# Kernel optimization log

Hardware: AMD Instinct MI355X
Metric: run time of the kernel (lower is better)

The kernel has to match this reference:

```python
import jax, jax.numpy as jnp
import numpy as np

T0, TBAR, TPOINTS, STEP = 0.0, 2.0, 10, 0.1
N_GRID = int(np.ceil((TBAR - T0) / STEP)) + 1  # 21 internal RK4 grid points (torchdiffeq fixed-grid)
B, N, D_IN, D_HID, D_FF, D_MLP, D_OUT = 256, 100, 3, 256, 1024, 128, 2


def _linear_params(key, fan_in, fan_out):
    # torch.nn.Linear default init: U(-1/sqrt(fan_in), 1/sqrt(fan_in))
    bound = 1.0 / np.sqrt(fan_in)
    kw, kb = jax.random.split(key)
    W = jax.random.uniform(kw, (fan_out, fan_in), minval=-bound, maxval=bound, dtype=jnp.float32)
    b = jax.random.uniform(kb, (fan_out,), minval=-bound, maxval=bound, dtype=jnp.float32)
    return W, b


def setup_inputs() -> dict:
    key = jax.random.key(0)
    kx, k1, k2, k3, k4 = jax.random.split(key, 5)
    w1_W, w1_b = _linear_params(k1, D_IN, D_HID)
    w2_W, w2_b = _linear_params(k2, D_HID, D_FF)
    w3_W, w3_b = _linear_params(k3, D_FF + D_HID, D_MLP)
    out_W, out_b = _linear_params(k4, D_MLP, D_OUT)
    return dict(
        x=jax.random.normal(kx, (B, N, D_IN), dtype=jnp.float32),
        w1_W=w1_W, w1_b=w1_b,
        w2_W=w2_W, w2_b=w2_b,
        w3_W=w3_W, w3_b=w3_b,
        out_W=out_W, out_b=out_b,
        wpool_w=jnp.ones((TPOINTS,), dtype=jnp.float32),
    )


def reference(x, w1_W, w1_b, w2_W, w2_b, w3_W, w3_b, out_W, out_b, wpool_w):
    feature = jax.nn.relu(x @ w1_W.T + w1_b)              # [B, N, 256]
    gamma = feature

    def f(p):  # nmODE dynamics (time-independent)
        return -p + jnp.sin(p + gamma) ** 2

    h = jnp.float32(STEP)

    def rk4_step(y, _):
        k1 = f(y)
        k2 = f(y + 0.5 * h * k1)
        k3 = f(y + 0.5 * h * k2)
        k4 = f(y + h * k3)
        y1 = y + (h / 6.0) * (k1 + 2.0 * k2 + 2.0 * k3 + k4)
        return y1, y1

    y0 = jnp.zeros_like(feature)
    _, ys_tail = jax.lax.scan(rk4_step, y0, None, length=N_GRID - 1)
    ys = jnp.concatenate([y0[None], ys_tail], axis=0)     # [21, B, N, 256]

    # torchdiffeq interpolates fixed-grid solution linearly at the requested timepoints
    tt = np.linspace(T0, TBAR, TPOINTS)
    pos = tt / STEP
    idx = np.minimum(np.floor(pos).astype(np.int32), N_GRID - 2)
    frac = (pos - idx).astype(np.float32)[:, None, None, None]
    yt = ys[idx] * (1.0 - frac) + ys[idx + 1] * frac      # [10, B, N, 256]

    # WeightedAveragePooling over timepoints
    w = jax.nn.softmax(wpool_w)
    yt = jnp.einsum('t,tbnd->bnd', w, yt)                 # [B, N, 256]

    x2 = jax.nn.relu(feature @ w2_W.T + w2_b)             # [B, N, 1024]
    x2 = jnp.max(x2, axis=1, keepdims=True)               # [B, 1, 1024]
    x2 = jnp.broadcast_to(x2, (x2.shape[0], feature.shape[1], x2.shape[2]))
    h3 = jax.nn.relu(jnp.concatenate([x2, yt], axis=2) @ w3_W.T + w3_b)  # [B, N, 128]
    return h3 @ out_W.T + out_b                           # [B, N, 2]
```

## Files before the change

### kernel.cpp

```cpp
#include <hip/hip_runtime.h>

typedef __bf16 bf16x8 __attribute__((ext_vector_type(8)));
typedef float f32x4 __attribute__((ext_vector_type(4)));
typedef unsigned short u16x8 __attribute__((ext_vector_type(8)));

#define MFMA16(a, b, c) __builtin_amdgcn_mfma_f32_16x16x32_bf16((a), (b), (c), 0, 0, 0)

#define BN_ROWS 25600
#define INVPI 0.31830988618379067f
#define TBL_N 4096
#define TBL_SCALE 409.6f
#define TBL_STEP (10.f / 4096.f)

__device__ __forceinline__ unsigned short f2bf(float f) {
    unsigned int u = __float_as_uint(f);
    u = u + 0x7FFFu + ((u >> 16) & 1u);
    return (unsigned short)(u >> 16);
}

__device__ __forceinline__ float feval(float y, float gp) {
    float u = fmaf(y, INVPI, gp);
    float cc = __builtin_amdgcn_cosf(u);
    return fmaf(-0.5f, cc, 0.5f - y);
}

__global__ void k_prep(const float* __restrict__ w2W, const float* __restrict__ w3W,
                       const float* __restrict__ wp,
                       unsigned short* __restrict__ w2bf, unsigned short* __restrict__ w3bbf,
                       float* __restrict__ tbl, float* __restrict__ w3aT) {
    int blk = blockIdx.x;
    if (blk < 128) {
        int i = (blk * 256 + threadIdx.x) * 8;
        const float4* s4 = reinterpret_cast<const float4*>(w2W + i);
        float4 a = s4[0], b = s4[1];
        u16x8 o;
        o[0] = f2bf(a.x); o[1] = f2bf(a.y); o[2] = f2bf(a.z); o[3] = f2bf(a.w);
        o[4] = f2bf(b.x); o[5] = f2bf(b.y); o[6] = f2bf(b.z); o[7] = f2bf(b.w);
        *reinterpret_cast<u16x8*>(w2bf + i) = o;
        return;
    }
    if (blk < 144) {
        int idx = ((blk - 128) * 256 + threadIdx.x) * 8;
        int j = idx >> 8, dk = idx & 255;
        const float4* s4 = reinterpret_cast<const float4*>(w3W + j * 1280 + 1024 + dk);
        float4 a = s4[0], b = s4[1];
        u16x8 o;
        o[0] = f2bf(a.x); o[1] = f2bf(a.y); o[2] = f2bf(a.z); o[3] = f2bf(a.w);
        o[4] = f2bf(b.x); o[5] = f2bf(b.y); o[6] = f2bf(b.z); o[7] = f2bf(b.w);
        *reinterpret_cast<u16x8*>(w3bbf + idx) = o;
        return;
    }
    if (blk < 160) {
        int gid = (blk - 144) * 256 + threadIdx.x;

        float c[21];
#pragma unroll
        for (int g = 0; g < 21; ++g) c[g] = 0.f;
        {
            float wv[10];
#pragma unroll
            for (int t = 0; t < 10; ++t) wv[t] = wp[t];
            float m = wv[0];
#pragma unroll
            for (int t = 1; t < 10; ++t) m = fmaxf(m, wv[t]);
            float s = 0.f;
#pragma unroll
            for (int t = 0; t < 10; ++t) { wv[t] = __expf(wv[t] - m); s += wv[t]; }
            float inv = 1.f / s;
            const int   idxs[10]  = {0, 2, 4, 6, 8, 11, 13, 15, 17, 19};
            const float fracs[10] = {0.f, 0.22222222f, 0.44444445f, 0.6666667f, 0.8888889f,
                                     0.11111111f, 0.33333334f, 0.5555556f, 0.7777778f, 1.0f};
#pragma unroll
            for (int t = 0; t < 10; ++t) {
                float w = wv[t] * inv;
                c[idxs[t]]     += w * (1.f - fracs[t]);
                c[idxs[t] + 1] += w * fracs[t];
            }
        }

        float gamma = gid * TBL_STEP;
        float gp = gamma * INVPI;
        float y = 0.f, acc = 0.f;
#pragma unroll
        for (int st = 0; st < 20; ++st) {
            float k1 = feval(y, gp);
            float k2 = feval(fmaf(0.05f, k1, y), gp);
            float k3 = feval(fmaf(0.05f, k2, y), gp);
            float k4 = feval(fmaf(0.1f,  k3, y), gp);
            float sm = k1 + k4;
            sm = fmaf(2.f, k2, sm);
            sm = fmaf(2.f, k3, sm);
            y  = fmaf(0.1f / 6.0f, sm, y);
            acc = fmaf(c[st + 1], y, acc);
        }
        tbl[gid] = acc;
        return;
    }
    {
        int i = (blk - 160) * 256 + threadIdx.x;
        int c = i & 1023, j = i >> 10;
        w3aT[c * 128 + j] = w3W[j * 1280 + c];
    }
}

__global__ void __launch_bounds__(256) k_feat(
    const float* __restrict__ x, const float* __restrict__ w1W, const float* __restrict__ w1b,
    const float* __restrict__ tbl,
    unsigned short* __restrict__ featbf, unsigned short* __restrict__ ytbf) {

    __shared__ float tl[TBL_N];
    {
        const float4* g4 = reinterpret_cast<const float4*>(tbl);
        float4* l4 = reinterpret_cast<float4*>(tl);
#pragma unroll
        for (int r = 0; r < 4; ++r) l4[r * 256 + threadIdx.x] = g4[r * 256 + threadIdx.x];
    }
    __syncthreads();

    int tid  = blockIdx.x * 256 + threadIdx.x;
    int base = tid * 8;
    int row  = base >> 8;
    int d0   = base & 255;

    float x0 = x[row * 3 + 0], x1 = x[row * 3 + 1], x2v = x[row * 3 + 2];

    float wreg[24];
    {
        const float4* w4 = reinterpret_cast<const float4*>(w1W + d0 * 3);
#pragma unroll
        for (int q = 0; q < 6; ++q) *reinterpret_cast<float4*>(&wreg[q * 4]) = w4[q];
    }
    float bb[8];
    {
        const float4* b4 = reinterpret_cast<const float4*>(w1b + d0);
        *reinterpret_cast<float4*>(&bb[0]) = b4[0];
        *reinterpret_cast<float4*>(&bb[4]) = b4[1];
    }

    u16x8 fbv, ybv;
#pragma unroll
    for (int j = 0; j < 8; ++j) {
        float g = fmaf(x0, wreg[j * 3], fmaf(x1, wreg[j * 3 + 1], fmaf(x2v, wreg[j * 3 + 2], bb[j])));
        g = fmaxf(g, 0.f);
        fbv[j] = f2bf(g);
        float t = g * TBL_SCALE;
        int i = (int)t;
        i = (i > TBL_N - 2) ? (TBL_N - 2) : i;
        float fr = t - (float)i;
        float a = tl[i], b = tl[i + 1];
        ybv[j] = f2bf(fmaf(fr, b - a, a));
    }
    *reinterpret_cast<u16x8*>(featbf + base) = fbv;
    *reinterpret_cast<u16x8*>(ytbf + base) = ybv;
}

__global__ void __launch_bounds__(256, 2) k_gemm2max(
    const unsigned short* __restrict__ featbf, const unsigned short* __restrict__ w2bf,
    const float* __restrict__ w2bias, const float* __restrict__ w3aT,
    float* __restrict__ vpart) {

    __shared__ __align__(1024) char smem[57344];

    int p = blockIdx.x;
    int xcd = p & 7, slot = p >> 3;
    int b = xcd * 32 + (slot >> 2);
    int q = slot & 3;

    int wave = threadIdx.x >> 6, lane = threadIdx.x & 63;
    int col16 = lane & 15, krow = lane >> 4;
    int colbase = q * 256 + wave * 64;

    const unsigned short* bp = w2bf + (size_t)(colbase + col16) * 256 + krow * 8;
    bf16x8 Bcur[4], Bnxt[4];
#pragma unroll
    for (int ct = 0; ct < 4; ++ct)
        Bcur[ct] = *reinterpret_cast<const bf16x8*>(bp + ct * 4096);

    {
        const unsigned short* src = featbf + (size_t)b * 25600;
        int r_in_pair = lane >> 5;
        int chp = lane & 31;
#pragma unroll
        for (int k = 0; k < 14; ++k) {
            int pr = wave + k * 4;
            int row = pr * 2 + r_in_pair;
            if (pr < 50) {
                int ch = chp ^ (row & 7);
                const unsigned short* g = src + row * 256 + ch * 8;
                __builtin_amdgcn_global_load_lds(
                    (const __attribute__((address_space(1))) void*)g,
                    (__attribute__((address_space(3))) void*)(smem + pr * 1024),
                    16, 0, 0);
            } else {
                *reinterpret_cast<f32x4*>(smem + pr * 1024 + lane * 16) = (f32x4){0.f,0.f,0.f,0.f};
            }
        }
    }
    __syncthreads();

    int sw = (col16 & 7) << 4;

    f32x4 acc[7][4];
#pragma unroll
    for (int mt = 0; mt < 7; ++mt)
#pragma unroll
        for (int ct = 0; ct < 4; ++ct) acc[mt][ct] = (f32x4){0.f, 0.f, 0.f, 0.f};

    const char* Ab = (const char*)smem;
#pragma unroll
    for (int k0 = 0; k0 < 8; ++k0) {
        int off = (k0 * 64 + krow * 16) ^ sw;
        bf16x8 Af[7];
#pragma unroll
        for (int mt = 0; mt < 7; ++mt)
            Af[mt] = *reinterpret_cast<const bf16x8*>(Ab + (mt * 16 + col16) * 512 + off);
        if (k0 < 7) {
#pragma unroll
            for (int ct = 0; ct < 4; ++ct)
                Bnxt[ct] = *reinterpret_cast<const bf16x8*>(bp + ct * 4096 + (k0 + 1) * 32);
        }
#pragma unroll
        for (int mt = 0; mt < 7; ++mt)
#pragma unroll
            for (int ct = 0; ct < 4; ++ct)
                acc[mt][ct] = MFMA16(Af[mt], Bcur[ct], acc[mt][ct]);
#pragma unroll
        for (int ct = 0; ct < 4; ++ct) Bcur[ct] = Bnxt[ct];
    }

    float bias[4], m[4];
#pragma unroll
    for (int ct = 0; ct < 4; ++ct) {
        bias[ct] = w2bias[colbase + ct * 16 + col16];
        m[ct] = 0.f;
    }
#pragma unroll
    for (int mt = 0; mt < 7; ++mt) {
#pragma unroll
        for (int r = 0; r < 4; ++r) {
            int n = mt * 16 + krow * 4 + r;
            bool valid = n < 100;
#pragma unroll
            for (int ct = 0; ct < 4; ++ct) {
                float v = fmaxf(acc[mt][ct][r] + bias[ct], 0.f);
                if (valid) m[ct] = fmaxf(m[ct], v);
            }
        }
    }
#pragma unroll
    for (int ct = 0; ct < 4; ++ct) {
        m[ct] = fmaxf(m[ct], __shfl_xor(m[ct], 16));
        m[ct] = fmaxf(m[ct], __shfl_xor(m[ct], 32));
    }

    float* xs = (float*)smem;
    float* p0s = xs + 256;
    float* p1s = xs + 384;

    __syncthreads();
    if (lane < 16) {
#pragma unroll
        for (int ct = 0; ct < 4; ++ct)
            xs[wave * 64 + ct * 16 + lane] = m[ct];
    }
    __syncthreads();

    {
        int j = (wave & 1) * 64 + lane;
        int ch = wave >> 1;
        const float* wt = w3aT + (size_t)(q * 256 + ch * 128) * 128 + j;
        float s0 = 0.f, s1 = 0.f;
#pragma unroll 8
        for (int c = 0; c < 128; c += 2) {
            s0 = fmaf(xs[ch * 128 + c],     wt[(size_t)c * 128],       s0);
            s1 = fmaf(xs[ch * 128 + c + 1], wt[(size_t)(c + 1) * 128], s1);
        }
        float* dst = (ch == 0) ? p0s : p1s;
        dst[j] = s0 + s1;
    }
    __syncthreads();
    if (threadIdx.x < 128)
        vpart[(size_t)b * 512 + q * 128 + threadIdx.x] = p0s[threadIdx.x] + p1s[threadIdx.x];
}

__global__ void __launch_bounds__(256) k_final(
    const unsigned short* __restrict__ ytbf, const unsigned short* __restrict__ w3bbf,
    const float* __restrict__ vpart, const float* __restrict__ w3bias,
    const float* __restrict__ outW, const float* __restrict__ outb,
    float* __restrict__ out) {

    __shared__ float h3s[32][132];
    int rbase = blockIdx.x * 32;
    int wave = threadIdx.x >> 6, lane = threadIdx.x & 63;
    int col16 = lane & 15, krow = lane >> 4;

    const unsigned short* ap0 = ytbf + (size_t)(rbase + col16) * 256 + krow * 8;
    const unsigned short* ap1 = ap0 + 16 * 256;
    const unsigned short* bp0 = w3bbf + (size_t)(wave * 32 + col16) * 256 + krow * 8;
    const unsigned short* bp1 = bp0 + 16 * 256;

    f32x4 a00 = {0.f,0.f,0.f,0.f}, a01 = {0.f,0.f,0.f,0.f};
    f32x4 a10 = {0.f,0.f,0.f,0.f}, a11 = {0.f,0.f,0.f,0.f};
#pragma unroll
    for (int k0 = 0; k0 < 8; ++k0) {
        bf16x8 A0 = *reinterpret_cast<const bf16x8*>(ap0 + k0 * 32);
        bf16x8 A1 = *reinterpret_cast<const bf16x8*>(ap1 + k0 * 32);
        bf16x8 B0 = *reinterpret_cast<const bf16x8*>(bp0 + k0 * 32);
        bf16x8 B1 = *reinterpret_cast<const bf16x8*>(bp1 + k0 * 32);
        a00 = MFMA16(A0, B0, a00);
        a01 = MFMA16(A0, B1, a01);
        a10 = MFMA16(A1, B0, a10);
        a11 = MFMA16(A1, B1, a11);
    }

#pragma unroll
    for (int mt = 0; mt < 2; ++mt) {
#pragma unroll
        for (int nt = 0; nt < 2; ++nt) {
            f32x4 acc = (mt == 0) ? ((nt == 0) ? a00 : a01) : ((nt == 0) ? a10 : a11);
#pragma unroll
            for (int r = 0; r < 4; ++r) {
                int rloc  = mt * 16 + krow * 4 + r;
                int rglob = rbase + rloc;
                int bb    = rglob / 100;
                int col   = wave * 32 + nt * 16 + col16;
                const float* vp = vpart + (size_t)bb * 512;
                float vsum = (vp[col] + vp[128 + col]) + (vp[256 + col] + vp[384 + col]);
                float h = acc[r] + vsum + w3bias[col];
                h3s[rloc][col] = fmaxf(h, 0.f);
            }
        }
    }
    __syncthreads();

    int r  = threadIdx.x >> 3;
    int jg = threadIdx.x & 7;
    float p0 = 0.f, p1 = 0.f;
#pragma unroll
    for (int t = 0; t < 16; ++t) {
        int j = jg * 16 + t;
        float h = h3s[r][j];
        p0 = fmaf(h, outW[j], p0);
        p1 = fmaf(h, outW[128 + j], p1);
    }
    p0 += __shfl_xor(p0, 1); p0 += __shfl_xor(p0, 2); p0 += __shfl_xor(p0, 4);
    p1 += __shfl_xor(p1, 1); p1 += __shfl_xor(p1, 2); p1 += __shfl_xor(p1, 4);
    if (jg == 0) {
        int rg = rbase + r;
        out[rg * 2 + 0] = p0 + outb[0];
        out[rg * 2 + 1] = p1 + outb[1];
    }
}

extern "C" void kernel_launch(void* const* d_in, const int* in_sizes, int n_in,
                              void* d_out, int out_size, void* d_ws, size_t ws_size,
                              hipStream_t stream) {
    const float* x    = (const float*)d_in[0];
    const float* w1W  = (const float*)d_in[1];
    const float* w1b  = (const float*)d_in[2];
    const float* w2W  = (const float*)d_in[3];
    const float* w2b  = (const float*)d_in[4];
    const float* w3W  = (const float*)d_in[5];
    const float* w3b  = (const float*)d_in[6];
    const float* outW = (const float*)d_in[7];
    const float* outb = (const float*)d_in[8];
    const float* wp   = (const float*)d_in[9];
    float* out = (float*)d_out;

    char* ws = (char*)d_ws;
    unsigned short* featbf = (unsigned short*)(ws);
    unsigned short* ytbf   = (unsigned short*)(ws + 13107200);
    unsigned short* w2bf_  = (unsigned short*)(ws + 26214400);
    unsigned short* w3bbf_ = (unsigned short*)(ws + 26738688);
    float* tbl             = (float*)(ws + 26804224);
    float* vpart           = (float*)(ws + 26820608);
    float* w3aT            = (float*)(ws + 27344896);

    k_prep<<<672, 256, 0, stream>>>(w2W, w3W, wp, w2bf_, w3bbf_, tbl, w3aT);
    k_feat<<<3200, 256, 0, stream>>>(x, w1W, w1b, tbl, featbf, ytbf);
    k_gemm2max<<<1024, 256, 0, stream>>>(featbf, w2bf_, w2b, w3aT, vpart);
    k_final<<<800, 256, 0, stream>>>(ytbf, w3bbf_, vpart, w3b, outW, outb, out);
}
```

Measured before the change: 70.37 us.

## Fuse feature, gemm-max, and final stages into one per-batch kernel

Replaces the three kernels k_feat, k_gemm2max and k_final with a single k_batch kernel that runs one 512-thread block per batch element. Features and the interpolated ODE values are computed directly into swizzled LDS, and both GEMMs and the output projection read from there. This removes the global round trips for featbf, ytbf and vpart and two kernel launches. In exchange there are only 256 large blocks using about 140KB of LDS each, which lowers occupancy and parallelism on a GPU with many CUs.

```diff
diff --git a/kernel.cpp b/kernel.cpp
--- a/kernel.cpp
+++ b/kernel.cpp
@@ -6,7 +6,6 @@
 
 #define MFMA16(a, b, c) __builtin_amdgcn_mfma_f32_16x16x32_bf16((a), (b), (c), 0, 0, 0)
 
-#define BN_ROWS 25600
 #define INVPI 0.31830988618379067f
 #define TBL_N 4096
 #define TBL_SCALE 409.6f
@@ -103,252 +102,224 @@
     }
 }
 
-__global__ void __launch_bounds__(256) k_feat(
+__global__ void __launch_bounds__(512) k_batch(
     const float* __restrict__ x, const float* __restrict__ w1W, const float* __restrict__ w1b,
     const float* __restrict__ tbl,
-    unsigned short* __restrict__ featbf, unsigned short* __restrict__ ytbf) {
-
+    const unsigned short* __restrict__ w2bf, const float* __restrict__ w2b,
+    const float* __restrict__ w3aT, const float* __restrict__ w3b,
+    const unsigned short* __restrict__ w3bbf,
+    const float* __restrict__ outW, const float* __restrict__ outb,
+    float* __restrict__ out) {
+
+    __shared__ __align__(1024) char smemA[57344];
+    __shared__ __align__(1024) char smemY[57344];
     __shared__ float tl[TBL_N];
+    __shared__ float w1s[1024];
+    __shared__ float xs[1024];
+    __shared__ float ps[4][128];
+    __shared__ float vs[128];
+    __shared__ float ps2[4][128][2];
+
+    const int b = blockIdx.x;
+    const int t = threadIdx.x;
+
     {
         const float4* g4 = reinterpret_cast<const float4*>(tbl);
         float4* l4 = reinterpret_cast<float4*>(tl);
-#pragma unroll
-        for (int r = 0; r < 4; ++r) l4[r * 256 + threadIdx.x] = g4[r * 256 + threadIdx.x];
-    }
-    __syncthreads();
-
-    int tid  = blockIdx.x * 256 + threadIdx.x;
-    int base = tid * 8;
-    int row  = base >> 8;
-    int d0   = base & 255;
-
-    float x0 = x[row * 3 + 0], x1 = x[row * 3 + 1], x2v = x[row * 3 + 2];
-
-    float wreg[24];
-    {
-        const float4* w4 = reinterpret_cast<const float4*>(w1W + d0 * 3);
-#pragma unroll
-        for (int q = 0; q < 6; ++q) *reinterpret_cast<float4*>(&wreg[q * 4]) = w4[q];
-    }
-    float bb[8];
-    {
-        const float4* b4 = reinterpret_cast<const float4*>(w1b + d0);
-        *reinterpret_cast<float4*>(&bb[0]) = b4[0];
-        *reinterpret_cast<float4*>(&bb[4]) = b4[1];
-    }
-
-    u16x8 fbv, ybv;
-#pragma unroll
-    for (int j = 0; j < 8; ++j) {
-        float g = fmaf(x0, wreg[j * 3], fmaf(x1, wreg[j * 3 + 1], fmaf(x2v, wreg[j * 3 + 2], bb[j])));
-        g = fmaxf(g, 0.f);
-        fbv[j] = f2bf(g);
-        float t = g * TBL_SCALE;
-        int i = (int)t;
-        i = (i > TBL_N - 2) ? (TBL_N - 2) : i;
-        float fr = t - (float)i;
-        float a = tl[i], b = tl[i + 1];
-        ybv[j] = f2bf(fmaf(fr, b - a, a));
-    }
-    *reinterpret_cast<u16x8*>(featbf + base) = fbv;
-    *reinterpret_cast<u16x8*>(ytbf + base) = ybv;
-}
-
-__global__ void __launch_bounds__(256, 2) k_gemm2max(
-    const unsigned short* __restrict__ featbf, const unsigned short* __restrict__ w2bf,
-    const float* __restrict__ w2bias, const float* __restrict__ w3aT,
-    float* __restrict__ vpart) {
-
-    __shared__ __align__(1024) char smem[57344];
-
-    int p = blockIdx.x;
-    int xcd = p & 7, slot = p >> 3;
-    int b = xcd * 32 + (slot >> 2);
-    int q = slot & 3;
-
-    int wave = threadIdx.x >> 6, lane = threadIdx.x & 63;
-    int col16 = lane & 15, krow = lane >> 4;
-    int colbase = q * 256 + wave * 64;
-
-    const unsigned short* bp = w2bf + (size_t)(colbase + col16) * 256 + krow * 8;
-    bf16x8 Bcur[4], Bnxt[4];
-#pragma unroll
-    for (int ct = 0; ct < 4; ++ct)
-        Bcur[ct] = *reinterpret_cast<const bf16x8*>(bp + ct * 4096);
-
-    {
-        const unsigned short* src = featbf + (size_t)b * 25600;
-        int r_in_pair = lane >> 5;
-        int chp = lane & 31;
-#pragma unroll
-        for (int k = 0; k < 14; ++k) {
-            int pr = wave + k * 4;
-            int row = pr * 2 + r_in_pair;
-            if (pr < 50) {
-                int ch = chp ^ (row & 7);
-                const unsigned short* g = src + row * 256 + ch * 8;
-                __builtin_amdgcn_global_load_lds(
-                    (const __attribute__((address_space(1))) void*)g,
-                    (__attribute__((address_space(3))) void*)(smem + pr * 1024),
-                    16, 0, 0);
+        l4[t] = g4[t];
+        l4[t + 512] = g4[t + 512];
+        if (t < 192)
+            reinterpret_cast<float4*>(w1s)[t] = reinterpret_cast<const float4*>(w1W)[t];
+        else if (t >= 256 && t < 320)
+            reinterpret_cast<float4*>(w1s + 768)[t - 256] =
+                reinterpret_cast<const float4*>(w1b)[t - 256];
+    }
+    __syncthreads();
+
+    {
+        const float* xb = x + (size_t)b * 300;
+#pragma unroll
+        for (int i = 0; i < 7; ++i) {
+            int k = t + i * 512;
+            int row = k >> 5, ch = k & 31;
+            int byte = row * 512 + ((ch * 16) ^ ((row & 7) << 4));
+            if (row < 100) {
+                float x0 = xb[row * 3], x1 = xb[row * 3 + 1], x2 = xb[row * 3 + 2];
+                int d0 = ch * 8;
+                u16x8 fv, yv;
+#pragma unroll
+                for (int j = 0; j < 8; ++j) {
+                    int d = d0 + j;
+                    float g = fmaf(x0, w1s[d * 3],
+                              fmaf(x1, w1s[d * 3 + 1],
+                              fmaf(x2, w1s[d * 3 + 2], w1s[768 + d])));
+                    g = fmaxf(g, 0.f);
+                    fv[j] = f2bf(g);
+                    float tt = g * TBL_SCALE;
+                    int ii = (int)tt;
+                    ii = (ii > TBL_N - 2) ? (TBL_N - 2) : ii;
+                    float fr = tt - (float)ii;
+                    float a0 = tl[ii], a1 = tl[ii + 1];
+                    yv[j] = f2bf(fmaf(fr, a1 - a0, a0));
+                }
+                *reinterpret_cast<u16x8*>(smemA + byte) = fv;
+                *reinterpret_cast<u16x8*>(smemY + byte) = yv;
             } else {
-                *reinterpret_cast<f32x4*>(smem + pr * 1024 + lane * 16) = (f32x4){0.f,0.f,0.f,0.f};
-            }
-        }
-    }
-    __syncthreads();
-
-    int sw = (col16 & 7) << 4;
-
-    f32x4 acc[7][4];
-#pragma unroll
-    for (int mt = 0; mt < 7; ++mt)
-#pragma unroll
-        for (int ct = 0; ct < 4; ++ct) acc[mt][ct] = (f32x4){0.f, 0.f, 0.f, 0.f};
-
-    const char* Ab = (const char*)smem;
-#pragma unroll
-    for (int k0 = 0; k0 < 8; ++k0) {
-        int off = (k0 * 64 + krow * 16) ^ sw;
-        bf16x8 Af[7];
+                *reinterpret_cast<f32x4*>(smemA + byte) = (f32x4){0.f, 0.f, 0.f, 0.f};
+                *reinterpret_cast<f32x4*>(smemY + byte) = (f32x4){0.f, 0.f, 0.f, 0.f};
+            }
+        }
+    }
+    __syncthreads();
+
+    const int wave = t >> 6, lane = t & 63;
+    const int col16 = lane & 15, krow = lane >> 4;
+    const int sw = (col16 & 7) << 4;
+
+#pragma unroll 1
+    for (int q = 0; q < 2; ++q) {
+        int colbase = q * 512 + wave * 64;
+        const unsigned short* bp = w2bf + (size_t)(colbase + col16) * 256 + krow * 8;
+
+        f32x4 acc[7][4];
 #pragma unroll
         for (int mt = 0; mt < 7; ++mt)
-            Af[mt] = *reinterpret_cast<const bf16x8*>(Ab + (mt * 16 + col16) * 512 + off);
-        if (k0 < 7) {
+#pragma unroll
+            for (int ct = 0; ct < 4; ++ct) acc[mt][ct] = (f32x4){0.f, 0.f, 0.f, 0.f};
+
+        bf16x8 Bcur[4], Bnxt[4];
+#pragma unroll
+        for (int ct = 0; ct < 4; ++ct)
+            Bcur[ct] = *reinterpret_cast<const bf16x8*>(bp + ct * 4096);
+
+#pragma unroll
+        for (int k0 = 0; k0 < 8; ++k0) {
+            int off = (k0 * 64 + krow * 16) ^ sw;
+            bf16x8 Af[7];
+#pragma unroll
+            for (int mt = 0; mt < 7; ++mt)
+                Af[mt] = *reinterpret_cast<const bf16x8*>(smemA + (mt * 16 + col16) * 512 + off);
+            if (k0 < 7) {
+#pragma unroll
+                for (int ct = 0; ct < 4; ++ct)
+                    Bnxt[ct] = *reinterpret_cast<const bf16x8*>(bp + ct * 4096 + (k0 + 1) * 32);
+            }
+#pragma unroll
+            for (int mt = 0; mt < 7; ++mt)
+#pragma unroll
+                for (int ct = 0; ct < 4; ++ct)
+                    acc[mt][ct] = MFMA16(Af[mt], Bcur[ct], acc[mt][ct]);
+#pragma unroll
+            for (int ct = 0; ct < 4; ++ct) Bcur[ct] = Bnxt[ct];
+        }
+
+        float bias[4], m[4];
+#pragma unroll
+        for (int ct = 0; ct < 4; ++ct) {
+            bias[ct] = w2b[colbase + ct * 16 + col16];
+            m[ct] = 0.f;
+        }
+#pragma unroll
+        for (int mt = 0; mt < 7; ++mt) {
+#pragma unroll
+            for (int r = 0; r < 4; ++r) {
+                bool valid = (mt * 16 + krow * 4 + r) < 100;
+#pragma unroll
+                for (int ct = 0; ct < 4; ++ct) {
+                    float v = fmaxf(acc[mt][ct][r] + bias[ct], 0.f);
+                    if (valid) m[ct] = fmaxf(m[ct], v);
+                }
+            }
+        }
+#pragma unroll
+        for (int ct = 0; ct < 4; ++ct) {
+            m[ct] = fmaxf(m[ct], __shfl_xor(m[ct], 16));
+            m[ct] = fmaxf(m[ct], __shfl_xor(m[ct], 32));
+        }
+        if (lane < 16) {
 #pragma unroll
             for (int ct = 0; ct < 4; ++ct)
-                Bnxt[ct] = *reinterpret_cast<const bf16x8*>(bp + ct * 4096 + (k0 + 1) * 32);
-        }
-#pragma unroll
-        for (int mt = 0; mt < 7; ++mt)
-#pragma unroll
-            for (int ct = 0; ct < 4; ++ct)
-                acc[mt][ct] = MFMA16(Af[mt], Bcur[ct], acc[mt][ct]);
-#pragma unroll
-        for (int ct = 0; ct < 4; ++ct) Bcur[ct] = Bnxt[ct];
-    }
-
-    float bias[4], m[4];
-#pragma unroll
-    for (int ct = 0; ct < 4; ++ct) {
-        bias[ct] = w2bias[colbase + ct * 16 + col16];
-        m[ct] = 0.f;
-    }
-#pragma unroll
-    for (int mt = 0; mt < 7; ++mt) {
-#pragma unroll
-        for (int r = 0; r < 4; ++r) {
-            int n = mt * 16 + krow * 4 + r;
-            bool valid = n < 100;
-#pragma unroll
-            for (int ct = 0; ct < 4; ++ct) {
-                float v = fmaxf(acc[mt][ct][r] + bias[ct], 0.f);
-                if (valid) m[ct] = fmaxf(m[ct], v);
-            }
-        }
-    }
-#pragma unroll
-    for (int ct = 0; ct < 4; ++ct) {
-        m[ct] = fmaxf(m[ct], __shfl_xor(m[ct], 16));
-        m[ct] = fmaxf(m[ct], __shfl_xor(m[ct], 32));
-    }
-
-    float* xs = (float*)smem;
-    float* p0s = xs + 256;
-    float* p1s = xs + 384;
-
-    __syncthreads();
-    if (lane < 16) {
-#pragma unroll
-        for (int ct = 0; ct < 4; ++ct)
-            xs[wave * 64 + ct * 16 + lane] = m[ct];
-    }
-    __syncthreads();
-
-    {
-        int j = (wave & 1) * 64 + lane;
-        int ch = wave >> 1;
-        const float* wt = w3aT + (size_t)(q * 256 + ch * 128) * 128 + j;
+                xs[colbase + ct * 16 + lane] = m[ct];
+        }
+    }
+    __syncthreads();
+
+    {
+        int j = t & 127, cq = t >> 7;
+        const float* wt = w3aT + (size_t)cq * 256 * 128 + j;
+        const float* xc = xs + cq * 256;
         float s0 = 0.f, s1 = 0.f;
 #pragma unroll 8
-        for (int c = 0; c < 128; c += 2) {
-            s0 = fmaf(xs[ch * 128 + c],     wt[(size_t)c * 128],       s0);
-            s1 = fmaf(xs[ch * 128 + c + 1], wt[(size_t)(c + 1) * 128], s1);
-        }
-        float* dst = (ch == 0) ? p0s : p1s;
-        dst[j] = s0 + s1;
-    }
-    __syncthreads();
-    if (threadIdx.x < 128)
-        vpart[(size_t)b * 512 + q * 128 + threadIdx.x] = p0s[threadIdx.x] + p1s[threadIdx.x];
-}
-
-__global__ void __launch_bounds__(256) k_final(
-    const unsigned short* __restrict__ ytbf, const unsigned short* __restrict__ w3bbf,
-    const float* __restrict__ vpart, const float* __restrict__ w3bias,
-    const float* __restrict__ outW, const float* __restrict__ outb,
-    float* __restrict__ out) {
-
-    __shared__ float h3s[32][132];
-    int rbase = blockIdx.x * 32;
-    int wave = threadIdx.x >> 6, lane = threadIdx.x & 63;
-    int col16 = lane & 15, krow = lane >> 4;
-
-    const unsigned short* ap0 = ytbf + (size_t)(rbase + col16) * 256 + krow * 8;
-    const unsigned short* ap1 = ap0 + 16 * 256;
-    const unsigned short* bp0 = w3bbf + (size_t)(wave * 32 + col16) * 256 + krow * 8;
-    const unsigned short* bp1 = bp0 + 16 * 256;
-
-    f32x4 a00 = {0.f,0.f,0.f,0.f}, a01 = {0.f,0.f,0.f,0.f};
-    f32x4 a10 = {0.f,0.f,0.f,0.f}, a11 = {0.f,0.f,0.f,0.f};
-#pragma unroll
-    for (int k0 = 0; k0 < 8; ++k0) {
-        bf16x8 A0 = *reinterpret_cast<const bf16x8*>(ap0 + k0 * 32);
-        bf16x8 A1 = *reinterpret_cast<const bf16x8*>(ap1 + k0 * 32);
-        bf16x8 B0 = *reinterpret_cast<const bf16x8*>(bp0 + k0 * 32);
-        bf16x8 B1 = *reinterpret_cast<const bf16x8*>(bp1 + k0 * 32);
-        a00 = MFMA16(A0, B0, a00);
-        a01 = MFMA16(A0, B1, a01);
-        a10 = MFMA16(A1, B0, a10);
-        a11 = MFMA16(A1, B1, a11);
-    }
-
-#pragma unroll
-    for (int mt = 0; mt < 2; ++mt) {
-#pragma unroll
-        for (int nt = 0; nt < 2; ++nt) {
-            f32x4 acc = (mt == 0) ? ((nt == 0) ? a00 : a01) : ((nt == 0) ? a10 : a11);
+        for (int c = 0; c < 256; c += 2) {
+            s0 = fmaf(xc[c],     wt[(size_t)c * 128],       s0);
+            s1 = fmaf(xc[c + 1], wt[(size_t)(c + 1) * 128], s1);
+        }
+        ps[cq][j] = s0 + s1;
+    }
+    __syncthreads();
+    if (t < 128)
+        vs[t] = ((ps[0][t] + ps[1][t]) + (ps[2][t] + ps[3][t])) + w3b[t];
+
+    f32x4 hacc[7];
+#pragma unroll
+    for (int mt = 0; mt < 7; ++mt) hacc[mt] = (f32x4){0.f, 0.f, 0.f, 0.f};
+    {
+        const unsigned short* bp4 = w3bbf + (size_t)(wave * 16 + col16) * 256 + krow * 8;
+        bf16x8 B4cur = *reinterpret_cast<const bf16x8*>(bp4);
+        bf16x8 B4nxt;
+#pragma unroll
+        for (int k0 = 0; k0 < 8; ++k0) {
+            int off = (k0 * 64 + krow * 16) ^ sw;
+            bf16x8 Af[7];
+#pragma unroll
+            for (int mt = 0; mt < 7; ++mt)
+                Af[mt] = *reinterpret_cast<const bf16x8*>(smemY + (mt * 16 + col16) * 512 + off);
+            if (k0 < 7) B4nxt = *reinterpret_cast<const bf16x8*>(bp4 + (k0 + 1) * 32);
+#pragma unroll
+            for (int mt = 0; mt < 7; ++mt)
+                hacc[mt] = MFMA16(Af[mt], B4cur, hacc[mt]);
+            B4cur = B4nxt;
+        }
+    }
+    __syncthreads();
+
+    {
+        float* hs = reinterpret_cast<float*>(smemA);
+        int col = wave * 16 + col16;
+#pragma unroll
+        for (int mt = 0; mt < 7; ++mt) {
 #pragma unroll
             for (int r = 0; r < 4; ++r) {
-                int rloc  = mt * 16 + krow * 4 + r;
-                int rglob = rbase + rloc;
-                int bb    = rglob / 100;
-                int col   = wave * 32 + nt * 16 + col16;
-                const float* vp = vpart + (size_t)bb * 512;
-                float vsum = (vp[col] + vp[128 + col]) + (vp[256 + col] + vp[384 + col]);
-                float h = acc[r] + vsum + w3bias[col];
-                h3s[rloc][col] = fmaxf(h, 0.f);
-            }
-        }
-    }
-    __syncthreads();
-
-    int r  = threadIdx.x >> 3;
-    int jg = threadIdx.x & 7;
-    float p0 = 0.f, p1 = 0.f;
-#pragma unroll
-    for (int t = 0; t < 16; ++t) {
-        int j = jg * 16 + t;
-        float h = h3s[r][j];
-        p0 = fmaf(h, outW[j], p0);
-        p1 = fmaf(h, outW[128 + j], p1);
-    }
-    p0 += __shfl_xor(p0, 1); p0 += __shfl_xor(p0, 2); p0 += __shfl_xor(p0, 4);
-    p1 += __shfl_xor(p1, 1); p1 += __shfl_xor(p1, 2); p1 += __shfl_xor(p1, 4);
-    if (jg == 0) {
-        int rg = rbase + r;
-        out[rg * 2 + 0] = p0 + outb[0];
-        out[rg * 2 + 1] = p1 + outb[1];
+                int row = mt * 16 + krow * 4 + r;
+                float h = fmaxf(hacc[mt][r] + vs[col], 0.f);
+                hs[row * 128 + ((col + row) & 127)] = h;
+            }
+        }
+    }
+    __syncthreads();
+
+    {
+        const float* hs = reinterpret_cast<const float*>(smemA);
+        int rr = t & 127, half = t >> 7;
+        float p0 = 0.f, p1 = 0.f;
+        if (rr < 112) {
+            int j0 = half * 32;
+#pragma unroll
+            for (int u = 0; u < 32; ++u) {
+                int j = j0 + u;
+                float h = hs[rr * 128 + ((j + rr) & 127)];
+                p0 = fmaf(h, outW[j], p0);
+                p1 = fmaf(h, outW[128 + j], p1);
+            }
+        }
+        ps2[half][rr][0] = p0;
+        ps2[half][rr][1] = p1;
+    }
+    __syncthreads();
+    if (t < 200) {
+        int row = t >> 1, c = t & 1;
+        out[((size_t)b * 100 + row) * 2 + c] =
+            ((ps2[0][row][c] + ps2[1][row][c]) + (ps2[2][row][c] + ps2[3][row][c])) + outb[c];
     }
 }
 
@@ -368,16 +339,12 @@
     float* out = (float*)d_out;
 
     char* ws = (char*)d_ws;
-    unsigned short* featbf = (unsigned short*)(ws);
-    unsigned short* ytbf   = (unsigned short*)(ws + 13107200);
-    unsigned short* w2bf_  = (unsigned short*)(ws + 26214400);
-    unsigned short* w3bbf_ = (unsigned short*)(ws + 26738688);
-    float* tbl             = (float*)(ws + 26804224);
-    float* vpart           = (float*)(ws + 26820608);
-    float* w3aT            = (float*)(ws + 27344896);
+    unsigned short* w2bf_  = (unsigned short*)(ws);
+    unsigned short* w3bbf_ = (unsigned short*)(ws + 524288);
+    float* tbl             = (float*)(ws + 589824);
+    float* w3aT            = (float*)(ws + 606208);
 
     k_prep<<<672, 256, 0, stream>>>(w2W, w3W, wp, w2bf_, w3bbf_, tbl, w3aT);
-    k_feat<<<3200, 256, 0, stream>>>(x, w1W, w1b, tbl, featbf, ytbf);
-    k_gemm2max<<<1024, 256, 0, stream>>>(featbf, w2bf_, w2b, w3aT, vpart);
-    k_final<<<800, 256, 0, stream>>>(ytbf, w3bbf_, vpart, w3b, outW, outb, out);
-}
+    k_batch<<<256, 512, 0, stream>>>(x, w1W, w1b, tbl, w2bf_, w2b, w3aT, w3b,
+                                     w3bbf_, outW, outb, out);
+}
```

Measured after the change: 86.74 us. +23.3%, slower.

## Merge column-quarter blocks into one block per batch and fuse w3 matvec

Applied to the files above, without the earlier changes.

The max-pooled GEMM kernel now uses one block per batch item that loads the feature tile once and loops over all four column quarters, instead of four blocks each reloading the tile. The follow-on 1024x128 projection is done in full per block using shuffle reductions over the original w3 layout. This drops the transpose prep and the partial-sum combine in the final kernel. The risks are fewer blocks (256) and serial quarter processing, which lower parallelism and latency hiding.

```diff
diff --git a/kernel.cpp b/kernel.cpp
--- a/kernel.cpp
+++ b/kernel.cpp
@@ -6,7 +6,6 @@
 
 #define MFMA16(a, b, c) __builtin_amdgcn_mfma_f32_16x16x32_bf16((a), (b), (c), 0, 0, 0)
 
-#define BN_ROWS 25600
 #define INVPI 0.31830988618379067f
 #define TBL_N 4096
 #define TBL_SCALE 409.6f
@@ -27,7 +26,7 @@
 __global__ void k_prep(const float* __restrict__ w2W, const float* __restrict__ w3W,
                        const float* __restrict__ wp,
                        unsigned short* __restrict__ w2bf, unsigned short* __restrict__ w3bbf,
-                       float* __restrict__ tbl, float* __restrict__ w3aT) {
+                       float* __restrict__ tbl) {
     int blk = blockIdx.x;
     if (blk < 128) {
         int i = (blk * 256 + threadIdx.x) * 8;
@@ -50,7 +49,7 @@
         *reinterpret_cast<u16x8*>(w3bbf + idx) = o;
         return;
     }
-    if (blk < 160) {
+    {
         int gid = (blk - 144) * 256 + threadIdx.x;
 
         float c[21];
@@ -94,12 +93,6 @@
             acc = fmaf(c[st + 1], y, acc);
         }
         tbl[gid] = acc;
-        return;
-    }
-    {
-        int i = (blk - 160) * 256 + threadIdx.x;
-        int c = i & 1023, j = i >> 10;
-        w3aT[c * 128 + j] = w3W[j * 1280 + c];
     }
 }
 
@@ -154,27 +147,18 @@
     *reinterpret_cast<u16x8*>(ytbf + base) = ybv;
 }
 
-__global__ void __launch_bounds__(256, 2) k_gemm2max(
+__global__ void __launch_bounds__(256, 2) k_G(
     const unsigned short* __restrict__ featbf, const unsigned short* __restrict__ w2bf,
-    const float* __restrict__ w2bias, const float* __restrict__ w3aT,
-    float* __restrict__ vpart) {
-
-    __shared__ __align__(1024) char smem[57344];
-
-    int p = blockIdx.x;
-    int xcd = p & 7, slot = p >> 3;
-    int b = xcd * 32 + (slot >> 2);
-    int q = slot & 3;
-
-    int wave = threadIdx.x >> 6, lane = threadIdx.x & 63;
-    int col16 = lane & 15, krow = lane >> 4;
-    int colbase = q * 256 + wave * 64;
-
-    const unsigned short* bp = w2bf + (size_t)(colbase + col16) * 256 + krow * 8;
-    bf16x8 Bcur[4], Bnxt[4];
-#pragma unroll
-    for (int ct = 0; ct < 4; ++ct)
-        Bcur[ct] = *reinterpret_cast<const bf16x8*>(bp + ct * 4096);
+    const float* __restrict__ w2b, const float* __restrict__ w3W,
+    const float* __restrict__ w3b, float* __restrict__ vglob) {
+
+    __shared__ __align__(1024) char smemA[57344];
+    __shared__ float xs[1024];
+
+    const int b = blockIdx.x;
+    const int wave = threadIdx.x >> 6, lane = threadIdx.x & 63;
+    const int col16 = lane & 15, krow = lane >> 4;
+    const int sw = (col16 & 7) << 4;
 
     {
         const unsigned short* src = featbf + (size_t)b * 25600;
@@ -189,105 +173,103 @@
                 const unsigned short* g = src + row * 256 + ch * 8;
                 __builtin_amdgcn_global_load_lds(
                     (const __attribute__((address_space(1))) void*)g,
-                    (__attribute__((address_space(3))) void*)(smem + pr * 1024),
+                    (__attribute__((address_space(3))) void*)(smemA + pr * 1024),
                     16, 0, 0);
             } else {
-                *reinterpret_cast<f32x4*>(smem + pr * 1024 + lane * 16) = (f32x4){0.f,0.f,0.f,0.f};
+                *reinterpret_cast<f32x4*>(smemA + pr * 1024 + lane * 16) = (f32x4){0.f,0.f,0.f,0.f};
             }
         }
     }
     __syncthreads();
 
-    int sw = (col16 & 7) << 4;
-
-    f32x4 acc[7][4];
-#pragma unroll
-    for (int mt = 0; mt < 7; ++mt)
-#pragma unroll
-        for (int ct = 0; ct < 4; ++ct) acc[mt][ct] = (f32x4){0.f, 0.f, 0.f, 0.f};
-
-    const char* Ab = (const char*)smem;
-#pragma unroll
-    for (int k0 = 0; k0 < 8; ++k0) {
-        int off = (k0 * 64 + krow * 16) ^ sw;
-        bf16x8 Af[7];
+#pragma unroll 1
+    for (int q = 0; q < 4; ++q) {
+        int colbase = q * 256 + wave * 64;
+        const unsigned short* bp = w2bf + (size_t)(colbase + col16) * 256 + krow * 8;
+
+        f32x4 acc[7][4];
 #pragma unroll
         for (int mt = 0; mt < 7; ++mt)
-            Af[mt] = *reinterpret_cast<const bf16x8*>(Ab + (mt * 16 + col16) * 512 + off);
-        if (k0 < 7) {
+#pragma unroll
+            for (int ct = 0; ct < 4; ++ct) acc[mt][ct] = (f32x4){0.f, 0.f, 0.f, 0.f};
+
+        bf16x8 Bcur[4], Bnxt[4];
+#pragma unroll
+        for (int ct = 0; ct < 4; ++ct)
+            Bcur[ct] = *reinterpret_cast<const bf16x8*>(bp + ct * 4096);
+
+#pragma unroll
+        for (int k0 = 0; k0 < 8; ++k0) {
+            int off = (k0 * 64 + krow * 16) ^ sw;
+            if (k0 < 7) {
+#pragma unroll
+                for (int ct = 0; ct < 4; ++ct)
+                    Bnxt[ct] = *reinterpret_cast<const bf16x8*>(bp + ct * 4096 + (k0 + 1) * 32);
+            }
+#pragma unroll
+            for (int mt = 0; mt < 7; ++mt) {
+                bf16x8 Af = *reinterpret_cast<const bf16x8*>(smemA + (mt * 16 + col16) * 512 + off);
+#pragma unroll
+                for (int ct = 0; ct < 4; ++ct)
+                    acc[mt][ct] = MFMA16(Af, Bcur[ct], acc[mt][ct]);
+            }
+#pragma unroll
+            for (int ct = 0; ct < 4; ++ct) Bcur[ct] = Bnxt[ct];
+        }
+
+        float bias[4], m[4];
+#pragma unroll
+        for (int ct = 0; ct < 4; ++ct) {
+            bias[ct] = w2b[colbase + ct * 16 + col16];
+            m[ct] = 0.f;
+        }
+#pragma unroll
+        for (int mt = 0; mt < 7; ++mt) {
+#pragma unroll
+            for (int r = 0; r < 4; ++r) {
+                bool valid = (mt * 16 + krow * 4 + r) < 100;
+#pragma unroll
+                for (int ct = 0; ct < 4; ++ct) {
+                    float v = fmaxf(acc[mt][ct][r] + bias[ct], 0.f);
+                    if (valid) m[ct] = fmaxf(m[ct], v);
+                }
+            }
+        }
+#pragma unroll
+        for (int ct = 0; ct < 4; ++ct) {
+            m[ct] = fmaxf(m[ct], __shfl_xor(m[ct], 16));
+            m[ct] = fmaxf(m[ct], __shfl_xor(m[ct], 32));
+        }
+        if (lane < 16) {
 #pragma unroll
             for (int ct = 0; ct < 4; ++ct)
-                Bnxt[ct] = *reinterpret_cast<const bf16x8*>(bp + ct * 4096 + (k0 + 1) * 32);
-        }
-#pragma unroll
-        for (int mt = 0; mt < 7; ++mt)
-#pragma unroll
-            for (int ct = 0; ct < 4; ++ct)
-                acc[mt][ct] = MFMA16(Af[mt], Bcur[ct], acc[mt][ct]);
-#pragma unroll
-        for (int ct = 0; ct < 4; ++ct) Bcur[ct] = Bnxt[ct];
-    }
-
-    float bias[4], m[4];
-#pragma unroll
-    for (int ct = 0; ct < 4; ++ct) {
-        bias[ct] = w2bias[colbase + ct * 16 + col16];
-        m[ct] = 0.f;
-    }
-#pragma unroll
-    for (int mt = 0; mt < 7; ++mt) {
-#pragma unroll
-        for (int r = 0; r < 4; ++r) {
-            int n = mt * 16 + krow * 4 + r;
-            bool valid = n < 100;
-#pragma unroll
-            for (int ct = 0; ct < 4; ++ct) {
-                float v = fmaxf(acc[mt][ct][r] + bias[ct], 0.f);
-                if (valid) m[ct] = fmaxf(m[ct], v);
-            }
-        }
-    }
-#pragma unroll
-    for (int ct = 0; ct < 4; ++ct) {
-        m[ct] = fmaxf(m[ct], __shfl_xor(m[ct], 16));
-        m[ct] = fmaxf(m[ct], __shfl_xor(m[ct], 32));
-    }
-
-    float* xs = (float*)smem;
-    float* p0s = xs + 256;
-    float* p1s = xs + 384;
-
+                xs[colbase + ct * 16 + lane] = m[ct];
+        }
+    }
     __syncthreads();
-    if (lane < 16) {
-#pragma unroll
-        for (int ct = 0; ct < 4; ++ct)
-            xs[wave * 64 + ct * 16 + lane] = m[ct];
-    }
-    __syncthreads();
-
-    {
-        int j = (wave & 1) * 64 + lane;
-        int ch = wave >> 1;
-        const float* wt = w3aT + (size_t)(q * 256 + ch * 128) * 128 + j;
-        float s0 = 0.f, s1 = 0.f;
-#pragma unroll 8
-        for (int c = 0; c < 128; c += 2) {
-            s0 = fmaf(xs[ch * 128 + c],     wt[(size_t)c * 128],       s0);
-            s1 = fmaf(xs[ch * 128 + c + 1], wt[(size_t)(c + 1) * 128], s1);
-        }
-        float* dst = (ch == 0) ? p0s : p1s;
-        dst[j] = s0 + s1;
-    }
-    __syncthreads();
-    if (threadIdx.x < 128)
-        vpart[(size_t)b * 512 + q * 128 + threadIdx.x] = p0s[threadIdx.x] + p1s[threadIdx.x];
-}
-
-__global__ void __launch_bounds__(256) k_final(
+
+    {
+        int j = wave * 32;
+#pragma unroll 2
+        for (int jj = 0; jj < 32; ++jj, ++j) {
+            const float* wr = w3W + (size_t)j * 1280;
+            float s = 0.f;
+#pragma unroll
+            for (int cc = 0; cc < 16; ++cc) {
+                int c = cc * 64 + lane;
+                s = fmaf(xs[c], wr[c], s);
+            }
+            s += __shfl_xor(s, 1);  s += __shfl_xor(s, 2);  s += __shfl_xor(s, 4);
+            s += __shfl_xor(s, 8);  s += __shfl_xor(s, 16); s += __shfl_xor(s, 32);
+            if (lane == 0) vglob[(size_t)b * 128 + j] = s + w3b[j];
+        }
+    }
+}
+
+__global__ void __launch_bounds__(256) k_B(
     const unsigned short* __restrict__ ytbf, const unsigned short* __restrict__ w3bbf,
-    const float* __restrict__ vpart, const float* __restrict__ w3bias,
-    const float* __restrict__ outW, const float* __restrict__ outb,
-    float* __restrict__ out) {
+    const float* __restrict__ vglob, const float* __restrict__ outW,
+    const float* __restrict__ outb, float* __restrict__ out) {
 
     __shared__ float h3s[32][132];
     int rbase = blockIdx.x * 32;
@@ -324,9 +306,7 @@
                 int rglob = rbase + rloc;
                 int bb    = rglob / 100;
                 int col   = wave * 32 + nt * 16 + col16;
-                const float* vp = vpart + (size_t)bb * 512;
-                float vsum = (vp[col] + vp[128 + col]) + (vp[256 + col] + vp[384 + col]);
-                float h = acc[r] + vsum + w3bias[col];
+                float h = acc[r] + vglob[(size_t)bb * 128 + col];
                 h3s[rloc][col] = fmaxf(h, 0.f);
             }
         }
@@ -337,8 +317,8 @@
     int jg = threadIdx.x & 7;
     float p0 = 0.f, p1 = 0.f;
 #pragma unroll
-    for (int t = 0; t < 16; ++t) {
-        int j = jg * 16 + t;
+    for (int tt = 0; tt < 16; ++tt) {
+        int j = jg * 16 + tt;
         float h = h3s[r][j];
         p0 = fmaf(h, outW[j], p0);
         p1 = fmaf(h, outW[128 + j], p1);
@@ -373,11 +353,10 @@
     unsigned short* w2bf_  = (unsigned short*)(ws + 26214400);
     unsigned short* w3bbf_ = (unsigned short*)(ws + 26738688);
     float* tbl             = (float*)(ws + 26804224);
-    float* vpart           = (float*)(ws + 26820608);
-    float* w3aT            = (float*)(ws + 27344896);
-
-    k_prep<<<672, 256, 0, stream>>>(w2W, w3W, wp, w2bf_, w3bbf_, tbl, w3aT);
+    float* vglob           = (float*)(ws + 26820608);
+
+    k_prep<<<160, 256, 0, stream>>>(w2W, w3W, wp, w2bf_, w3bbf_, tbl);
     k_feat<<<3200, 256, 0, stream>>>(x, w1W, w1b, tbl, featbf, ytbf);
-    k_gemm2max<<<1024, 256, 0, stream>>>(featbf, w2bf_, w2b, w3aT, vpart);
-    k_final<<<800, 256, 0, stream>>>(ytbf, w3bbf_, vpart, w3b, outW, outb, out);
-}
+    k_G<<<256, 256, 0, stream>>>(featbf, w2bf_, w2b, w3W, w3b, vglob);
+    k_B<<<800, 256, 0, stream>>>(ytbf, w3bbf_, vglob, outW, outb, out);
+}
```

Result: slower. 113.8 us (+61.8%).
